# Kernel tuning notes

Hardware: AMD Instinct MI355X
Metric: run time of the kernel (lower is better)

The kernel has to match this reference:

```python
import jax, jax.numpy as jnp
import numpy as np

BATCH = 16384
STEPS = 32
LAT = 64
IN_W = STEPS * (2 * LAT + 1) + 2 * LAT  # 4256


def setup_inputs() -> dict:
    key = jax.random.key(0)
    k1, k2 = jax.random.split(key)
    inputs = jax.random.normal(k1, (BATCH, IN_W), dtype=jnp.float32) * 0.1
    noise = jax.random.normal(k2, (BATCH, LAT), dtype=jnp.float32)
    return {"inputs": inputs, "noise": noise, "flow_steps": STEPS, "latent_dim": LAT}


def reference(inputs, noise, flow_steps, latent_dim):
    S, L = flow_steps, latent_dim
    B = inputs.shape[0]
    q0_mu = inputs[:, :L]
    q0_logsigma2 = inputs[:, L:2 * L]
    z0 = q0_mu + noise * jnp.exp(0.5 * q0_logsigma2)  # reparam sample (B, L)
    # initial variational loss term (add_loss in original)
    kl0 = -0.5 * jnp.mean(jnp.sum(noise * noise, axis=-1) + jnp.sum(q0_logsigma2, axis=-1))
    # per-step flow params, laid out step-major for scan: (S, B, L) and (S, B)
    U = inputs[:, 2 * L:(2 + S) * L].reshape(B, S, L).transpose(1, 0, 2)
    W = inputs[:, (2 + S) * L:(2 + 2 * S) * L].reshape(B, S, L).transpose(1, 0, 2)
    b = inputs[:, (2 + 2 * S) * L:(2 + 2 * S) * L + S].T  # (S, B)

    def step(z, uwb):
        u, w, bb = uwb
        h = jnp.sum(w * z, axis=-1) + bb          # (B,)
        uw = jnp.sum(u * w, axis=-1)              # (B,)
        t = jnp.tanh(h)
        # log|det Jacobian| loss term (tanh activation branch)
        loss = -jnp.mean(jnp.log(jnp.abs((1.0 - t * t) * uw + 1.0)))
        z = z + u * t[:, None]
        return z, loss

    z, losses = jax.lax.scan(step, z0, (U, W, b))
    total_loss = kl0 + jnp.sum(losses)
    return z, total_loss
```

## Files before the change

### kernel.cpp

```cpp
#include <hip/hip_runtime.h>
#include <math.h>


constexpr int BATCH = 16384;
constexpr int STEPS = 32;
constexpr int LAT   = 64;
constexpr int IN_W  = STEPS * (2 * LAT + 1) + 2 * LAT;

template <int CTRL>
__device__ __forceinline__ float dpp_mov(float x) {
    return __int_as_float(
        __builtin_amdgcn_update_dpp(0, __float_as_int(x), CTRL, 0xF, 0xF, true));
}

__device__ __forceinline__ float wave_reduce_to63(float x) {
    x += dpp_mov<0x111>(x);
    x += dpp_mov<0x112>(x);
    x += dpp_mov<0x114>(x);
    x += dpp_mov<0x118>(x);
    x += dpp_mov<0x142>(x);
    x += dpp_mov<0x143>(x);
    return x;
}

__device__ __forceinline__ float bcast63(float x) {
    return __int_as_float(__builtin_amdgcn_readlane(__float_as_int(x), 63));
}

__global__ __launch_bounds__(256)
void planar_flow_kernel(const float* __restrict__ inputs,
                        const float* __restrict__ noise,
                        float* __restrict__ z_out,
                        float* __restrict__ loss_out)
{
    const int lane = threadIdx.x & 63;
    const int wv   = threadIdx.x >> 6;
    const int row  = (blockIdx.x << 2) + wv;

    const float* rp = inputs + (size_t)row * IN_W;

    float mu  = rp[lane];
    float ls2 = rp[LAT + lane];
    float nz  = noise[(size_t)row * LAT + lane];
    float bvec = rp[2 * LAT + 2 * STEPS * LAT + (lane & 31)];

    float z = mu + nz * __expf(0.5f * ls2);

    float kl = wave_reduce_to63(nz * nz + ls2);
    float acc = -0.5f * kl;

    const float* up = rp + 2 * LAT;
    const float* wp = rp + 2 * LAT + STEPS * LAT;

    #pragma unroll 8
    for (int s = 0; s < STEPS; ++s) {
        float u = up[s * LAT + lane];
        float w = wp[s * LAT + lane];

        float hv = wave_reduce_to63(w * z);
        float bs = __int_as_float(__builtin_amdgcn_readlane(__float_as_int(bvec), s));
        float h  = bcast63(hv) + bs;

        float uwv = wave_reduce_to63(u * w);

        float e = __expf(2.0f * h);
        float t = 1.0f - 2.0f * __builtin_amdgcn_rcpf(e + 1.0f);

        acc -= __logf(fabsf((1.0f - t * t) * uwv + 1.0f));

        z += u * t;
    }

    z_out[(size_t)row * LAT + lane] = z;

    __shared__ float partial[4];
    if (lane == 63) partial[wv] = acc;
    __syncthreads();
    if (threadIdx.x == 0) {
        float s = (partial[0] + partial[1] + partial[2] + partial[3]) * (1.0f / BATCH);
        atomicAdd(loss_out, s);
    }
}

extern "C" void kernel_launch(void* const* d_in, const int* in_sizes, int n_in,
                              void* d_out, int out_size, void* d_ws, size_t ws_size,
                              hipStream_t stream)
{
    const float* inputs = (const float*)d_in[0];
    const float* noise  = (const float*)d_in[1];
    float* z_out    = (float*)d_out;
    float* loss_out = (float*)d_out + (size_t)BATCH * LAT;

    hipMemsetAsync(loss_out, 0, sizeof(float), stream);

    planar_flow_kernel<<<dim3(BATCH / 4), dim3(256), 0, stream>>>(
        inputs, noise, z_out, loss_out);
}
```

Measured before the change: 384.8 us.

## Map four rows per wavefront with float4 loads and 16-lane DPP reductions

Each wavefront now handles four batch rows: every 16-lane group owns one row, and each lane holds four latent elements loaded as float4. Per-step dot products become local 4-wide FMAs followed by a 4-stage row-level DPP reduction, replacing the 6-stage full-wave reduction and readlane broadcast. Per-step biases are staged through shared memory. The aim is fewer cross-lane ops per row and wider memory transactions. The trade-offs are a quarter as many blocks and some redundant per-lane log computations, which the final reduction corrects by scaling by an extra 1/16.

```diff
diff --git a/kernel.cpp b/kernel.cpp
--- a/kernel.cpp
+++ b/kernel.cpp
@@ -13,6 +13,14 @@
         __builtin_amdgcn_update_dpp(0, __float_as_int(x), CTRL, 0xF, 0xF, true));
 }
 
+__device__ __forceinline__ float rowsum16(float x) {
+    x += dpp_mov<0x121>(x);
+    x += dpp_mov<0x122>(x);
+    x += dpp_mov<0x124>(x);
+    x += dpp_mov<0x128>(x);
+    return x;
+}
+
 __device__ __forceinline__ float wave_reduce_to63(float x) {
     x += dpp_mov<0x111>(x);
     x += dpp_mov<0x112>(x);
@@ -23,10 +31,6 @@
     return x;
 }
 
-__device__ __forceinline__ float bcast63(float x) {
-    return __int_as_float(__builtin_amdgcn_readlane(__float_as_int(x), 63));
-}
-
 __global__ __launch_bounds__(256)
 void planar_flow_kernel(const float* __restrict__ inputs,
                         const float* __restrict__ noise,
@@ -35,49 +39,69 @@
 {
     const int lane = threadIdx.x & 63;
     const int wv   = threadIdx.x >> 6;
-    const int row  = (blockIdx.x << 2) + wv;
+    const int g    = lane >> 4;
+    const int i    = lane & 15;
+
+    const int row = (((blockIdx.x << 2) + wv) << 2) + g;
 
     const float* rp = inputs + (size_t)row * IN_W;
 
-    float mu  = rp[lane];
-    float ls2 = rp[LAT + lane];
-    float nz  = noise[(size_t)row * LAT + lane];
-    float bvec = rp[2 * LAT + 2 * STEPS * LAT + (lane & 31)];
+    __shared__ float sb[4 * 128];
 
-    float z = mu + nz * __expf(0.5f * ls2);
+    const float4 mu  = *(const float4*)(rp + 4 * i);
+    const float4 ls2 = *(const float4*)(rp + LAT + 4 * i);
+    const float4 nz  = *(const float4*)(noise + (size_t)row * LAT + 4 * i);
 
-    float kl = wave_reduce_to63(nz * nz + ls2);
-    float acc = -0.5f * kl;
+    const float* bp = rp + 2 * LAT + 2 * STEPS * LAT;
+    sb[wv * 128 + i * 4 + g]        = bp[i];
+    sb[wv * 128 + (i + 16) * 4 + g] = bp[i + 16];
+    __syncthreads();
 
-    const float* up = rp + 2 * LAT;
-    const float* wp = rp + 2 * LAT + STEPS * LAT;
+    float4 z;
+    z.x = fmaf(nz.x, __expf(0.5f * ls2.x), mu.x);
+    z.y = fmaf(nz.y, __expf(0.5f * ls2.y), mu.y);
+    z.z = fmaf(nz.z, __expf(0.5f * ls2.z), mu.z);
+    z.w = fmaf(nz.w, __expf(0.5f * ls2.w), mu.w);
+
+    float klp = nz.x * nz.x + nz.y * nz.y + nz.z * nz.z + nz.w * nz.w
+              + ls2.x + ls2.y + ls2.z + ls2.w;
+    float acc = -0.5f * rowsum16(klp);
+
+    const float* up  = rp + 2 * LAT;
+    const float* wp  = rp + 2 * LAT + STEPS * LAT;
+    const float* sbp = sb + wv * 128 + g;
 
     #pragma unroll 8
     for (int s = 0; s < STEPS; ++s) {
-        float u = up[s * LAT + lane];
-        float w = wp[s * LAT + lane];
+        const float4 u = *(const float4*)(up + s * LAT + 4 * i);
+        const float4 w = *(const float4*)(wp + s * LAT + 4 * i);
 
-        float hv = wave_reduce_to63(w * z);
-        float bs = __int_as_float(__builtin_amdgcn_readlane(__float_as_int(bvec), s));
-        float h  = bcast63(hv) + bs;
+        float hp = w.x * z.x + w.y * z.y + w.z * z.z + w.w * z.w;
+        float h  = rowsum16(hp) + sbp[s * 4];
 
-        float uwv = wave_reduce_to63(u * w);
+        float uwp = u.x * w.x + u.y * w.y + u.z * w.z + u.w * w.w;
+        float uw  = rowsum16(uwp);
 
         float e = __expf(2.0f * h);
         float t = 1.0f - 2.0f * __builtin_amdgcn_rcpf(e + 1.0f);
 
-        acc -= __logf(fabsf((1.0f - t * t) * uwv + 1.0f));
+        acc -= __logf(fabsf(fmaf(1.0f - t * t, uw, 1.0f)));
 
-        z += u * t;
+        z.x = fmaf(u.x, t, z.x);
+        z.y = fmaf(u.y, t, z.y);
+        z.z = fmaf(u.z, t, z.z);
+        z.w = fmaf(u.w, t, z.w);
     }
 
-    z_out[(size_t)row * LAT + lane] = z;
+    *(float4*)(z_out + (size_t)row * LAT + 4 * i) = z;
 
     __shared__ float partial[4];
-    if (lane == 63) partial[wv] = acc;
+    float wsum = wave_reduce_to63(acc);
+    if (lane == 63) partial[wv] = wsum;
     __syncthreads();
     if (threadIdx.x == 0) {
-        float s = (partial[0] + partial[1] + partial[2] + partial[3]) * (1.0f / BATCH);
+        float s = (partial[0] + partial[1] + partial[2] + partial[3])
+                * (1.0f / (16.0f * BATCH));
         atomicAdd(loss_out, s);
     }
 }
@@ -93,6 +117,6 @@
 
     hipMemsetAsync(loss_out, 0, sizeof(float), stream);
 
-    planar_flow_kernel<<<dim3(BATCH / 4), dim3(256), 0, stream>>>(
+    planar_flow_kernel<<<dim3(BATCH / 16), dim3(256), 0, stream>>>(
         inputs, noise, z_out, loss_out);
 }
```

Result: no change. 383.5 us (-0.4%).
